# Optimization experiments

Hardware: AMD Instinct MI355X
Metric: run time of the kernel (lower is better)

Reference implementation:

```python
import jax, jax.numpy as jnp
import numpy as np

ATOM_FDIM = 35
BOND_FDIM = 5
MAX_NB = 15
HIDDEN = 512
DEPTH = 6
N_MOLS = 1024
ATOMS_PER_MOL = 32
N_ATOMS = N_MOLS * ATOMS_PER_MOL      # 32768
N_BONDS = 2 * N_ATOMS                  # 65536 (each bond appears in both directions)
N_MESS = 8192                          # tree messages (row 0 is the zero pad slot)
TOTAL_MSG = N_MESS + N_BONDS           # index space for agraph/bgraph


def setup_inputs() -> dict:
    key = jax.random.key(0)
    ks = jax.random.split(key, 8)
    fatoms = jax.random.normal(ks[0], (N_ATOMS, ATOM_FDIM), jnp.float32)
    fbonds = jax.random.normal(ks[1], (N_BONDS, ATOM_FDIM + BOND_FDIM), jnp.float32)
    agraph = jax.random.randint(ks[2], (N_ATOMS, MAX_NB), 0, TOTAL_MSG, dtype=jnp.int32)
    bgraph = jax.random.randint(ks[3], (N_BONDS, MAX_NB), 0, TOTAL_MSG, dtype=jnp.int32)
    # row 0 of the concatenated message table is the padding slot -> zero it
    tree_message = jax.random.normal(ks[4], (N_MESS, HIDDEN), jnp.float32).at[0].set(0.0)
    starts = jnp.arange(N_MOLS, dtype=jnp.int32) * ATOMS_PER_MOL
    scope = jnp.stack([starts, jnp.full((N_MOLS,), ATOMS_PER_MOL, jnp.int32)], axis=1)
    s_i = 1.0 / np.sqrt(ATOM_FDIM + BOND_FDIM)
    s_h = 1.0 / np.sqrt(HIDDEN)
    s_o = 1.0 / np.sqrt(ATOM_FDIM + HIDDEN)
    W_i = jax.random.normal(ks[5], (ATOM_FDIM + BOND_FDIM, HIDDEN), jnp.float32) * s_i
    W_h = jax.random.normal(ks[6], (HIDDEN, HIDDEN), jnp.float32) * s_h
    W_o = jax.random.normal(ks[7], (ATOM_FDIM + HIDDEN, HIDDEN), jnp.float32) * s_o
    b_o = jnp.zeros((HIDDEN,), jnp.float32)
    return {"fatoms": fatoms, "fbonds": fbonds, "agraph": agraph, "bgraph": bgraph,
            "scope": scope, "tree_message": tree_message,
            "W_i": W_i, "W_h": W_h, "W_o": W_o, "b_o": b_o}


def reference(fatoms, fbonds, agraph, bgraph, scope, tree_message, W_i, W_h, W_o, b_o):
    binput = fbonds @ W_i                         # [B, H]
    graph_message = jax.nn.relu(binput)

    def step(gm, _):
        message = jnp.concatenate([tree_message, gm], axis=0)   # [M+B, H]
        nei = message[bgraph].sum(axis=1)                       # gather-sum [B, H]
        return jax.nn.relu(binput + nei @ W_h), None

    graph_message, _ = jax.lax.scan(step, graph_message, None, length=DEPTH - 1)

    message = jnp.concatenate([tree_message, graph_message], axis=0)
    nei = message[agraph].sum(axis=1)             # [A, H]
    ainput = jnp.concatenate([fatoms, nei], axis=1)
    atom_hiddens = jax.nn.relu(ainput @ W_o + b_o)

    # scope is uniform (st = i*ATOMS_PER_MOL, le = ATOMS_PER_MOL) -> static segment ids
    seg = jnp.repeat(jnp.arange(N_MOLS), ATOMS_PER_MOL)
    sums = jax.ops.segment_sum(atom_hiddens, seg, num_segments=N_MOLS)
    return sums / scope[:, 1:].astype(atom_hiddens.dtype)
```

## Files before the change

kernel.cpp:

```cpp
#include <hip/hip_runtime.h>
#include <stdint.h>


#define MAX_NB 15
#define HID 512
#define NA 32768
#define NB 65536
#define NMESS 8192

typedef unsigned short u16;
typedef unsigned int u32;
typedef __bf16 bf16x8 __attribute__((ext_vector_type(8)));
typedef float f32x4 __attribute__((ext_vector_type(4)));

__device__ __forceinline__ u16 f2bf(float f) {
  u32 u = __builtin_bit_cast(u32, f);
  u32 r = (u + 0x7fffu + ((u >> 16) & 1u)) >> 16;
  return (u16)r;
}
__device__ __forceinline__ float bf2f(u16 b) {
  u32 u = ((u32)b) << 16;
  return __builtin_bit_cast(float, u);
}
__device__ __forceinline__ float bflo(u32 u) {
  return __builtin_bit_cast(float, u << 16);
}
__device__ __forceinline__ float bfhi(u32 u) {
  return __builtin_bit_cast(float, u & 0xffff0000u);
}

__device__ __forceinline__ void async16(const u16* g, u16* l) {
  __builtin_amdgcn_global_load_lds(
      (const __attribute__((address_space(1))) u32*)g,
      (__attribute__((address_space(3))) u32*)l, 16, 0, 0);
}

__global__ __launch_bounds__(256) void prep_kernel(
    const float* __restrict__ fbonds, const float* __restrict__ tree,
    const float* __restrict__ Wi, const float* __restrict__ Wh,
    const float* __restrict__ Wo, u16* __restrict__ msg,
    u16* __restrict__ fbpad, u16* __restrict__ wi_t, u16* __restrict__ wh_t,
    u16* __restrict__ wo_t) {
  int t = blockIdx.x * 256 + threadIdx.x;
  const int N0 = NMESS * HID;
  const int N1 = NB * 64;
  const int N2 = 512 * 64;
  const int N3 = 512 * 512;
  const int N4 = 512 * 576;
  if (t < N0) { msg[t] = f2bf(tree[t]); return; }
  t -= N0;
  if (t < N1) {
    int row = t >> 6, c = t & 63;
    fbpad[t] = (c < 40) ? f2bf(fbonds[row * 40 + c]) : (u16)0;
    return;
  }
  t -= N1;
  if (t < N2) {
    int n = t >> 6, k = t & 63;
    wi_t[t] = (k < 40) ? f2bf(Wi[k * 512 + n]) : (u16)0;
    return;
  }
  t -= N2;
  if (t < N3) {
    int n = t >> 9, k = t & 511;
    wh_t[t] = f2bf(Wh[k * 512 + n]);
    return;
  }
  t -= N3;
  if (t < N4) {
    int n = t / 576, k = t - n * 576;
    float v = 0.f;
    if (k < 512) v = Wo[(35 + k) * 512 + n];
    else if (k < 547) v = Wo[(k - 512) * 512 + n];
    wo_t[t] = f2bf(v);
    return;
  }
}

__global__ __launch_bounds__(256) void gather_bonds(
    const u16* __restrict__ msg, const int* __restrict__ bgraph,
    u16* __restrict__ nei) {
  int row = blockIdx.x * 4 + (threadIdx.x >> 6);
  int lane = threadIdx.x & 63;
  const int* idxp = bgraph + row * MAX_NB;
  int ids[MAX_NB];
#pragma unroll
  for (int j = 0; j < MAX_NB; j++) ids[j] = idxp[j];
  const u16* base = msg + lane * 8;
  uint4 v[MAX_NB];
#pragma unroll
  for (int j = 0; j < MAX_NB; j++)
    v[j] = *(const uint4*)(base + (size_t)ids[j] * HID);
  float acc[8] = {0, 0, 0, 0, 0, 0, 0, 0};
#pragma unroll
  for (int j = 0; j < MAX_NB; j++) {
    acc[0] += bflo(v[j].x); acc[1] += bfhi(v[j].x);
    acc[2] += bflo(v[j].y); acc[3] += bfhi(v[j].y);
    acc[4] += bflo(v[j].z); acc[5] += bfhi(v[j].z);
    acc[6] += bflo(v[j].w); acc[7] += bfhi(v[j].w);
  }
  uint4 o;
  o.x = (u32)f2bf(acc[0]) | ((u32)f2bf(acc[1]) << 16);
  o.y = (u32)f2bf(acc[2]) | ((u32)f2bf(acc[3]) << 16);
  o.z = (u32)f2bf(acc[4]) | ((u32)f2bf(acc[5]) << 16);
  o.w = (u32)f2bf(acc[6]) | ((u32)f2bf(acc[7]) << 16);
  *(uint4*)(nei + (size_t)row * HID + lane * 8) = o;
}

__global__ __launch_bounds__(256) void gather_atoms(
    const u16* __restrict__ msg, const int* __restrict__ agraph,
    const float* __restrict__ fatoms, u16* __restrict__ ainput) {
  int row = blockIdx.x * 4 + (threadIdx.x >> 6);
  int lane = threadIdx.x & 63;
  const int* idxp = agraph + row * MAX_NB;
  int ids[MAX_NB];
#pragma unroll
  for (int j = 0; j < MAX_NB; j++) ids[j] = idxp[j];
  const u16* base = msg + lane * 8;
  uint4 v[MAX_NB];
#pragma unroll
  for (int j = 0; j < MAX_NB; j++)
    v[j] = *(const uint4*)(base + (size_t)ids[j] * HID);
  float acc[8] = {0, 0, 0, 0, 0, 0, 0, 0};
#pragma unroll
  for (int j = 0; j < MAX_NB; j++) {
    acc[0] += bflo(v[j].x); acc[1] += bfhi(v[j].x);
    acc[2] += bflo(v[j].y); acc[3] += bfhi(v[j].y);
    acc[4] += bflo(v[j].z); acc[5] += bfhi(v[j].z);
    acc[6] += bflo(v[j].w); acc[7] += bfhi(v[j].w);
  }
  uint4 o;
  o.x = (u32)f2bf(acc[0]) | ((u32)f2bf(acc[1]) << 16);
  o.y = (u32)f2bf(acc[2]) | ((u32)f2bf(acc[3]) << 16);
  o.z = (u32)f2bf(acc[4]) | ((u32)f2bf(acc[5]) << 16);
  o.w = (u32)f2bf(acc[6]) | ((u32)f2bf(acc[7]) << 16);
  u16* arow = ainput + (size_t)row * 576;
  *(uint4*)(arow + lane * 8) = o;
  float tv = (lane < 35) ? fatoms[(size_t)row * 35 + lane] : 0.f;
  arow[512 + lane] = f2bf(tv);
}

template <int EPI>
__global__ __launch_bounds__(256) void gemm_k(
    const u16* __restrict__ A, const u16* __restrict__ Bt, int K,
    u16* __restrict__ binput, u16* __restrict__ msgout,
    const float* __restrict__ bo, const int* __restrict__ scope,
    float* __restrict__ out) {
  __shared__ __align__(16) u16 As[128 * 32];
  __shared__ __align__(16) u16 Bs[128 * 32];
  const int t = threadIdx.x;
  const int lane = t & 63;
  const int w = t >> 6;
  const int wm = w & 1, wn = w >> 1;
  const int mBase = blockIdx.x * 128;
  const int nBase = blockIdx.y * 128;
  const int r = t >> 2;
  const int c8 = (t & 3) * 8;
  const int q8 = (lane >> 4) * 8;
  const int l15 = lane & 15;

  f32x4 acc[4][4];
#pragma unroll
  for (int i = 0; i < 4; i++)
#pragma unroll
    for (int j = 0; j < 4; j++)
#pragma unroll
      for (int rg = 0; rg < 4; rg++) acc[i][j][rg] = 0.f;

  for (int kb = 0; kb < K; kb += 32) {
    __syncthreads();
    async16(A + (size_t)(mBase + r) * K + kb + c8, As + r * 32 + c8);
    async16(A + (size_t)(mBase + r + 64) * K + kb + c8, As + (r + 64) * 32 + c8);
    async16(Bt + (size_t)(nBase + r) * K + kb + c8, Bs + r * 32 + c8);
    async16(Bt + (size_t)(nBase + r + 64) * K + kb + c8, Bs + (r + 64) * 32 + c8);
    __syncthreads();
    bf16x8 av[4], bv[4];
#pragma unroll
    for (int i = 0; i < 4; i++)
      av[i] = *(const bf16x8*)(As + (wm * 64 + i * 16 + l15) * 32 + q8);
#pragma unroll
    for (int j = 0; j < 4; j++)
      bv[j] = *(const bf16x8*)(Bs + (wn * 64 + j * 16 + l15) * 32 + q8);
#pragma unroll
    for (int i = 0; i < 4; i++)
#pragma unroll
      for (int j = 0; j < 4; j++)
        acc[i][j] = __builtin_amdgcn_mfma_f32_16x16x32_bf16(av[i], bv[j],
                                                            acc[i][j], 0, 0, 0);
  }

  if (EPI == 2) {
#pragma unroll
    for (int m = 0; m < 2; m++) {
      int mol = (mBase + wm * 64 + m * 32) >> 5;
      float inv_le = 1.0f / (float)scope[mol * 2 + 1];
#pragma unroll
      for (int j = 0; j < 4; j++) {
        int col = nBase + wn * 64 + j * 16 + l15;
        float bias = bo[col];
        float s = 0.f;
#pragma unroll
        for (int i = 2 * m; i < 2 * m + 2; i++)
#pragma unroll
          for (int rg = 0; rg < 4; rg++)
            s += fmaxf(acc[i][j][rg] + bias, 0.f);
        s += __shfl_xor(s, 16, 64);
        s += __shfl_xor(s, 32, 64);
        if (lane < 16) out[(size_t)mol * HID + col] = s * inv_le;
      }
    }
  } else {
#pragma unroll
    for (int i = 0; i < 4; i++) {
      int row = mBase + wm * 64 + i * 16 + (lane >> 4) * 4;
#pragma unroll
      for (int j = 0; j < 4; j++) {
        int col = nBase + wn * 64 + j * 16 + l15;
#pragma unroll
        for (int rg = 0; rg < 4; rg++) {
          float v = acc[i][j][rg];
          size_t gi = (size_t)(row + rg) * HID + col;
          if (EPI == 0) {
            binput[gi] = f2bf(v);
            msgout[gi + (size_t)NMESS * HID] = f2bf(fmaxf(v, 0.f));
          } else {
            v += bf2f(binput[gi]);
            msgout[gi + (size_t)NMESS * HID] = f2bf(fmaxf(v, 0.f));
          }
        }
      }
    }
  }
}

extern "C" void kernel_launch(void* const* d_in, const int* in_sizes, int n_in,
                              void* d_out, int out_size, void* d_ws,
                              size_t ws_size, hipStream_t stream) {
  const float* fatoms = (const float*)d_in[0];
  const float* fbonds = (const float*)d_in[1];
  const int* agraph = (const int*)d_in[2];
  const int* bgraph = (const int*)d_in[3];
  const int* scope = (const int*)d_in[4];
  const float* tree = (const float*)d_in[5];
  const float* Wi = (const float*)d_in[6];
  const float* Wh = (const float*)d_in[7];
  const float* Wo = (const float*)d_in[8];
  const float* bo = (const float*)d_in[9];
  float* out = (float*)d_out;

  char* ws = (char*)d_ws;
  u16* msg = (u16*)(ws);
  u16* binput = (u16*)(ws + 75497472ull);
  u16* nei = (u16*)(ws + 142606336ull);
  u16* wi_t = (u16*)(ws + 209715200ull);
  u16* wh_t = (u16*)(ws + 209780736ull);
  u16* wo_t = (u16*)(ws + 210305024ull);
  u16* fbpad = nei;
  u16* ainput = binput;

  prep_kernel<<<35072, 256, 0, stream>>>(fbonds, tree, Wi, Wh, Wo, msg, fbpad,
                                         wi_t, wh_t, wo_t);

  dim3 gB(NB / 128, 4);
  gemm_k<0><<<gB, 256, 0, stream>>>(fbpad, wi_t, 64, binput, msg, nullptr,
                                    nullptr, nullptr);
  for (int d = 0; d < 5; d++) {
    gather_bonds<<<NB / 4, 256, 0, stream>>>(msg, bgraph, nei);
    gemm_k<1><<<gB, 256, 0, stream>>>(nei, wh_t, 512, binput, msg, nullptr,
                                      nullptr, nullptr);
  }
  gather_atoms<<<NA / 4, 256, 0, stream>>>(msg, agraph, fatoms, ainput);
  dim3 gO(NA / 128, 4);
  gemm_k<2><<<gO, 256, 0, stream>>>(ainput, wo_t, 576, nullptr, nullptr, bo,
                                    scope, out);
}
```

Baseline: 1.295 ms.

## Gather via async global-to-LDS loads and remap GEMM blocks per XCD

Replaces the register-based gather kernels with a templated kernel that stages each neighbor row into shared memory using async16 direct-to-LDS loads. Each wave now handles four rows, loading them in two batches of 8 and 7. Separately, the GEMM grid becomes 1D, with block indices remapped so consecutive M tiles land on the same XCD, aiming for better L2 reuse of the A rows across the four N tiles. The gather waits with full waitcnt between batches, so it exposes less memory parallelism per wave than the original 15 outstanding loads.

```diff
diff --git a/kernel.cpp b/kernel.cpp
--- a/kernel.cpp
+++ b/kernel.cpp
@@ -77,83 +77,84 @@
   }
 }
 
-__global__ __launch_bounds__(256) void gather_bonds(
-    const u16* __restrict__ msg, const int* __restrict__ bgraph,
-    u16* __restrict__ nei) {
-  int row = blockIdx.x * 4 + (threadIdx.x >> 6);
-  int lane = threadIdx.x & 63;
-  const int* idxp = bgraph + row * MAX_NB;
-  int ids[MAX_NB];
-#pragma unroll
-  for (int j = 0; j < MAX_NB; j++) ids[j] = idxp[j];
-  const u16* base = msg + lane * 8;
-  uint4 v[MAX_NB];
-#pragma unroll
-  for (int j = 0; j < MAX_NB; j++)
-    v[j] = *(const uint4*)(base + (size_t)ids[j] * HID);
-  float acc[8] = {0, 0, 0, 0, 0, 0, 0, 0};
-#pragma unroll
-  for (int j = 0; j < MAX_NB; j++) {
-    acc[0] += bflo(v[j].x); acc[1] += bfhi(v[j].x);
-    acc[2] += bflo(v[j].y); acc[3] += bfhi(v[j].y);
-    acc[4] += bflo(v[j].z); acc[5] += bfhi(v[j].z);
-    acc[6] += bflo(v[j].w); acc[7] += bfhi(v[j].w);
-  }
-  uint4 o;
-  o.x = (u32)f2bf(acc[0]) | ((u32)f2bf(acc[1]) << 16);
-  o.y = (u32)f2bf(acc[2]) | ((u32)f2bf(acc[3]) << 16);
-  o.z = (u32)f2bf(acc[4]) | ((u32)f2bf(acc[5]) << 16);
-  o.w = (u32)f2bf(acc[6]) | ((u32)f2bf(acc[7]) << 16);
-  *(uint4*)(nei + (size_t)row * HID + lane * 8) = o;
-}
-
-__global__ __launch_bounds__(256) void gather_atoms(
-    const u16* __restrict__ msg, const int* __restrict__ agraph,
-    const float* __restrict__ fatoms, u16* __restrict__ ainput) {
-  int row = blockIdx.x * 4 + (threadIdx.x >> 6);
-  int lane = threadIdx.x & 63;
-  const int* idxp = agraph + row * MAX_NB;
-  int ids[MAX_NB];
-#pragma unroll
-  for (int j = 0; j < MAX_NB; j++) ids[j] = idxp[j];
-  const u16* base = msg + lane * 8;
-  uint4 v[MAX_NB];
-#pragma unroll
-  for (int j = 0; j < MAX_NB; j++)
-    v[j] = *(const uint4*)(base + (size_t)ids[j] * HID);
-  float acc[8] = {0, 0, 0, 0, 0, 0, 0, 0};
-#pragma unroll
-  for (int j = 0; j < MAX_NB; j++) {
-    acc[0] += bflo(v[j].x); acc[1] += bfhi(v[j].x);
-    acc[2] += bflo(v[j].y); acc[3] += bfhi(v[j].y);
-    acc[4] += bflo(v[j].z); acc[5] += bfhi(v[j].z);
-    acc[6] += bflo(v[j].w); acc[7] += bfhi(v[j].w);
-  }
-  uint4 o;
-  o.x = (u32)f2bf(acc[0]) | ((u32)f2bf(acc[1]) << 16);
-  o.y = (u32)f2bf(acc[2]) | ((u32)f2bf(acc[3]) << 16);
-  o.z = (u32)f2bf(acc[4]) | ((u32)f2bf(acc[5]) << 16);
-  o.w = (u32)f2bf(acc[6]) | ((u32)f2bf(acc[7]) << 16);
-  u16* arow = ainput + (size_t)row * 576;
-  *(uint4*)(arow + lane * 8) = o;
-  float tv = (lane < 35) ? fatoms[(size_t)row * 35 + lane] : 0.f;
-  arow[512 + lane] = f2bf(tv);
+template <int ATOMS>
+__global__ __launch_bounds__(256) void gather_dma(
+    const u16* __restrict__ msg, const int* __restrict__ graph,
+    const float* __restrict__ fatoms, u16* __restrict__ outbuf) {
+  __shared__ __align__(16) u16 sbuf[4][8][HID];
+  const int lane = threadIdx.x & 63;
+  const int w = threadIdx.x >> 6;
+  u16* buf = &sbuf[w][0][0];
+  const int rowBase = (blockIdx.x * 4 + w) * 4;
+  const int OSTRIDE = ATOMS ? 576 : HID;
+
+  for (int r = 0; r < 4; r++) {
+    const int row = rowBase + r;
+    const int* idxp = graph + row * MAX_NB;
+    int myid = (lane < MAX_NB) ? idxp[lane] : 0;
+    int ids[MAX_NB];
+#pragma unroll
+    for (int j = 0; j < MAX_NB; j++) ids[j] = __shfl(myid, j, 64);
+
+    float acc[8] = {0, 0, 0, 0, 0, 0, 0, 0};
+    __builtin_amdgcn_s_waitcnt(0);
+#pragma unroll
+    for (int j = 0; j < 8; j++)
+      async16(msg + (size_t)ids[j] * HID + lane * 8, buf + j * HID + lane * 8);
+    __builtin_amdgcn_s_waitcnt(0);
+#pragma unroll
+    for (int j = 0; j < 8; j++) {
+      uint4 v = *(const uint4*)(buf + j * HID + lane * 8);
+      acc[0] += bflo(v.x); acc[1] += bfhi(v.x);
+      acc[2] += bflo(v.y); acc[3] += bfhi(v.y);
+      acc[4] += bflo(v.z); acc[5] += bfhi(v.z);
+      acc[6] += bflo(v.w); acc[7] += bfhi(v.w);
+    }
+    __builtin_amdgcn_s_waitcnt(0);
+#pragma unroll
+    for (int j = 8; j < MAX_NB; j++)
+      async16(msg + (size_t)ids[j] * HID + lane * 8,
+              buf + (j - 8) * HID + lane * 8);
+    __builtin_amdgcn_s_waitcnt(0);
+#pragma unroll
+    for (int j = 8; j < MAX_NB; j++) {
+      uint4 v = *(const uint4*)(buf + (j - 8) * HID + lane * 8);
+      acc[0] += bflo(v.x); acc[1] += bfhi(v.x);
+      acc[2] += bflo(v.y); acc[3] += bfhi(v.y);
+      acc[4] += bflo(v.z); acc[5] += bfhi(v.z);
+      acc[6] += bflo(v.w); acc[7] += bfhi(v.w);
+    }
+    uint4 o;
+    o.x = (u32)f2bf(acc[0]) | ((u32)f2bf(acc[1]) << 16);
+    o.y = (u32)f2bf(acc[2]) | ((u32)f2bf(acc[3]) << 16);
+    o.z = (u32)f2bf(acc[4]) | ((u32)f2bf(acc[5]) << 16);
+    o.w = (u32)f2bf(acc[6]) | ((u32)f2bf(acc[7]) << 16);
+    u16* orow = outbuf + (size_t)row * OSTRIDE;
+    *(uint4*)(orow + lane * 8) = o;
+    if (ATOMS) {
+      float tv = (lane < 35) ? fatoms[(size_t)row * 35 + lane] : 0.f;
+      orow[512 + lane] = f2bf(tv);
+    }
+  }
 }
 
 template <int EPI>
 __global__ __launch_bounds__(256) void gemm_k(
-    const u16* __restrict__ A, const u16* __restrict__ Bt, int K,
+    const u16* __restrict__ A, const u16* __restrict__ Bt, int K, int mtx,
     u16* __restrict__ binput, u16* __restrict__ msgout,
     const float* __restrict__ bo, const int* __restrict__ scope,
     float* __restrict__ out) {
   __shared__ __align__(16) u16 As[128 * 32];
   __shared__ __align__(16) u16 Bs[128 * 32];
+  const int L = blockIdx.x;
+  const int xcd = L & 7;
+  const int q = L >> 3;
+  const int mBase = (xcd * mtx + (q >> 2)) * 128;
+  const int nBase = (q & 3) * 128;
   const int t = threadIdx.x;
   const int lane = t & 63;
   const int w = t >> 6;
   const int wm = w & 1, wn = w >> 1;
-  const int mBase = blockIdx.x * 128;
-  const int nBase = blockIdx.y * 128;
   const int r = t >> 2;
   const int c8 = (t & 3) * 8;
   const int q8 = (lane >> 4) * 8;
@@ -261,16 +262,14 @@
   prep_kernel<<<35072, 256, 0, stream>>>(fbonds, tree, Wi, Wh, Wo, msg, fbpad,
                                          wi_t, wh_t, wo_t);
 
-  dim3 gB(NB / 128, 4);
-  gemm_k<0><<<gB, 256, 0, stream>>>(fbpad, wi_t, 64, binput, msg, nullptr,
-                                    nullptr, nullptr);
+  gemm_k<0><<<2048, 256, 0, stream>>>(fbpad, wi_t, 64, 64, binput, msg,
+                                      nullptr, nullptr, nullptr);
   for (int d = 0; d < 5; d++) {
-    gather_bonds<<<NB / 4, 256, 0, stream>>>(msg, bgraph, nei);
-    gemm_k<1><<<gB, 256, 0, stream>>>(nei, wh_t, 512, binput, msg, nullptr,
-                                      nullptr, nullptr);
-  }
-  gather_atoms<<<NA / 4, 256, 0, stream>>>(msg, agraph, fatoms, ainput);
-  dim3 gO(NA / 128, 4);
-  gemm_k<2><<<gO, 256, 0, stream>>>(ainput, wo_t, 576, nullptr, nullptr, bo,
-                                    scope, out);
-}
+    gather_dma<0><<<NB / 16, 256, 0, stream>>>(msg, bgraph, nullptr, nei);
+    gemm_k<1><<<2048, 256, 0, stream>>>(nei, wh_t, 512, 64, binput, msg,
+                                        nullptr, nullptr, nullptr);
+  }
+  gather_dma<1><<<NA / 16, 256, 0, stream>>>(msg, agraph, fatoms, ainput);
+  gemm_k<2><<<1024, 256, 0, stream>>>(ainput, wo_t, 576, 32, nullptr, nullptr,
+                                      bo, scope, out);
+}
```

After: 1.274 ms. About the same (-1.7%).

## Remap block indices for XCD-local L2 locality and stream gather loads

Applied to the files above, without the earlier changes.

Gather and GEMM kernels remap the linear block index so that each of the 8 XCDs (blocks are dispatched round-robin across them) processes a contiguous range of rows. In the GEMMs, the four N-tiles of one M-tile then land on the same XCD and can share its L2 copy of the A panel. The gather kernels also switch from loading all 15 neighbor indices and vectors up front to a per-neighbor load-and-accumulate loop, which lowers register pressure at the cost of less explicit memory-level parallelism. The GEMM grid becomes 1-D and takes an extra tile-count parameter.

```diff
diff --git a/kernel.cpp b/kernel.cpp
--- a/kernel.cpp
+++ b/kernel.cpp
@@ -80,24 +80,20 @@
 __global__ __launch_bounds__(256) void gather_bonds(
     const u16* __restrict__ msg, const int* __restrict__ bgraph,
     u16* __restrict__ nei) {
-  int row = blockIdx.x * 4 + (threadIdx.x >> 6);
+  const int xcd = blockIdx.x & 7;
+  const int chunk = blockIdx.x >> 3;
+  int row = xcd * (NB / 8) + chunk * 4 + (threadIdx.x >> 6);
   int lane = threadIdx.x & 63;
   const int* idxp = bgraph + row * MAX_NB;
-  int ids[MAX_NB];
-#pragma unroll
-  for (int j = 0; j < MAX_NB; j++) ids[j] = idxp[j];
-  const u16* base = msg + lane * 8;
-  uint4 v[MAX_NB];
-#pragma unroll
-  for (int j = 0; j < MAX_NB; j++)
-    v[j] = *(const uint4*)(base + (size_t)ids[j] * HID);
   float acc[8] = {0, 0, 0, 0, 0, 0, 0, 0};
 #pragma unroll
   for (int j = 0; j < MAX_NB; j++) {
-    acc[0] += bflo(v[j].x); acc[1] += bfhi(v[j].x);
-    acc[2] += bflo(v[j].y); acc[3] += bfhi(v[j].y);
-    acc[4] += bflo(v[j].z); acc[5] += bfhi(v[j].z);
-    acc[6] += bflo(v[j].w); acc[7] += bfhi(v[j].w);
+    int id = idxp[j];
+    uint4 v = *(const uint4*)(msg + (size_t)id * HID + lane * 8);
+    acc[0] += bflo(v.x); acc[1] += bfhi(v.x);
+    acc[2] += bflo(v.y); acc[3] += bfhi(v.y);
+    acc[4] += bflo(v.z); acc[5] += bfhi(v.z);
+    acc[6] += bflo(v.w); acc[7] += bfhi(v.w);
   }
   uint4 o;
   o.x = (u32)f2bf(acc[0]) | ((u32)f2bf(acc[1]) << 16);
@@ -110,24 +106,20 @@
 __global__ __launch_bounds__(256) void gather_atoms(
     const u16* __restrict__ msg, const int* __restrict__ agraph,
     const float* __restrict__ fatoms, u16* __restrict__ ainput) {
-  int row = blockIdx.x * 4 + (threadIdx.x >> 6);
+  const int xcd = blockIdx.x & 7;
+  const int chunk = blockIdx.x >> 3;
+  int row = xcd * (NA / 8) + chunk * 4 + (threadIdx.x >> 6);
   int lane = threadIdx.x & 63;
   const int* idxp = agraph + row * MAX_NB;
-  int ids[MAX_NB];
-#pragma unroll
-  for (int j = 0; j < MAX_NB; j++) ids[j] = idxp[j];
-  const u16* base = msg + lane * 8;
-  uint4 v[MAX_NB];
-#pragma unroll
-  for (int j = 0; j < MAX_NB; j++)
-    v[j] = *(const uint4*)(base + (size_t)ids[j] * HID);
   float acc[8] = {0, 0, 0, 0, 0, 0, 0, 0};
 #pragma unroll
   for (int j = 0; j < MAX_NB; j++) {
-    acc[0] += bflo(v[j].x); acc[1] += bfhi(v[j].x);
-    acc[2] += bflo(v[j].y); acc[3] += bfhi(v[j].y);
-    acc[4] += bflo(v[j].z); acc[5] += bfhi(v[j].z);
-    acc[6] += bflo(v[j].w); acc[7] += bfhi(v[j].w);
+    int id = idxp[j];
+    uint4 v = *(const uint4*)(msg + (size_t)id * HID + lane * 8);
+    acc[0] += bflo(v.x); acc[1] += bfhi(v.x);
+    acc[2] += bflo(v.y); acc[3] += bfhi(v.y);
+    acc[4] += bflo(v.z); acc[5] += bfhi(v.z);
+    acc[6] += bflo(v.w); acc[7] += bfhi(v.w);
   }
   uint4 o;
   o.x = (u32)f2bf(acc[0]) | ((u32)f2bf(acc[1]) << 16);
@@ -142,18 +134,21 @@
 
 template <int EPI>
 __global__ __launch_bounds__(256) void gemm_k(
-    const u16* __restrict__ A, const u16* __restrict__ Bt, int K,
+    const u16* __restrict__ A, const u16* __restrict__ Bt, int K, int mtx,
     u16* __restrict__ binput, u16* __restrict__ msgout,
     const float* __restrict__ bo, const int* __restrict__ scope,
     float* __restrict__ out) {
   __shared__ __align__(16) u16 As[128 * 32];
   __shared__ __align__(16) u16 Bs[128 * 32];
+  const int L = blockIdx.x;
+  const int xcd = L & 7;
+  const int q = L >> 3;
+  const int mBase = (xcd * mtx + (q >> 2)) * 128;
+  const int nBase = (q & 3) * 128;
   const int t = threadIdx.x;
   const int lane = t & 63;
   const int w = t >> 6;
   const int wm = w & 1, wn = w >> 1;
-  const int mBase = blockIdx.x * 128;
-  const int nBase = blockIdx.y * 128;
   const int r = t >> 2;
   const int c8 = (t & 3) * 8;
   const int q8 = (lane >> 4) * 8;
@@ -261,16 +256,14 @@
   prep_kernel<<<35072, 256, 0, stream>>>(fbonds, tree, Wi, Wh, Wo, msg, fbpad,
                                          wi_t, wh_t, wo_t);
 
-  dim3 gB(NB / 128, 4);
-  gemm_k<0><<<gB, 256, 0, stream>>>(fbpad, wi_t, 64, binput, msg, nullptr,
-                                    nullptr, nullptr);
+  gemm_k<0><<<2048, 256, 0, stream>>>(fbpad, wi_t, 64, 64, binput, msg,
+                                      nullptr, nullptr, nullptr);
   for (int d = 0; d < 5; d++) {
     gather_bonds<<<NB / 4, 256, 0, stream>>>(msg, bgraph, nei);
-    gemm_k<1><<<gB, 256, 0, stream>>>(nei, wh_t, 512, binput, msg, nullptr,
-                                      nullptr, nullptr);
+    gemm_k<1><<<2048, 256, 0, stream>>>(nei, wh_t, 512, 64, binput, msg,
+                                        nullptr, nullptr, nullptr);
   }
   gather_atoms<<<NA / 4, 256, 0, stream>>>(msg, agraph, fatoms, ainput);
-  dim3 gO(NA / 128, 4);
-  gemm_k<2><<<gO, 256, 0, stream>>>(ainput, wo_t, 576, nullptr, nullptr, bo,
-                                    scope, out);
-}
+  gemm_k<2><<<1024, 256, 0, stream>>>(ainput, wo_t, 576, 32, nullptr, nullptr,
+                                      bo, scope, out);
+}
```

New measurement: 1.249 ms. -3.6%, faster.
